# Kernel tuning notes

Hardware: AMD Instinct MI355X
Metric: run time of the kernel (lower is better)

Reference implementation:

```python
import jax, jax.numpy as jnp
import numpy as np

HIDDEN = 1024
HEADS = 16
HEAD_DIM = HIDDEN // HEADS


def setup_inputs() -> dict:
    key = jax.random.key(0)
    ks = jax.random.split(key, 8)
    B, S = 2, 2048
    scale = 1.0 / np.sqrt(HIDDEN)
    inp = {
        "hidden_states": jax.random.normal(ks[0], (B, S, HIDDEN), dtype=jnp.float32),
        "attention_mask": jnp.zeros((B, 1, 1, S), dtype=jnp.float32),
        "q_w": jax.random.normal(ks[1], (HIDDEN, HIDDEN), dtype=jnp.float32) * scale,
        "q_b": jnp.zeros((HIDDEN,), dtype=jnp.float32),
        "k_w": jax.random.normal(ks[2], (HIDDEN, HIDDEN), dtype=jnp.float32) * scale,
        "k_b": jnp.zeros((HIDDEN,), dtype=jnp.float32),
        "v_w": jax.random.normal(ks[3], (HIDDEN, HIDDEN), dtype=jnp.float32) * scale,
        "v_b": jnp.zeros((HIDDEN,), dtype=jnp.float32),
    }
    return inp


def _split_heads(x):
    # [B, S, H] -> [B, heads, S, head_dim]
    B, S, _ = x.shape
    return x.reshape(B, S, HEADS, HEAD_DIM).transpose(0, 2, 1, 3)


def reference(hidden_states, attention_mask, q_w, q_b, k_w, k_b, v_w, v_b):
    # Linear projections (torch Linear: x @ W.T + b; here weights stored as [in, out])
    q = _split_heads(hidden_states @ q_w + q_b)  # [B, h, S, d]
    k = _split_heads(hidden_states @ k_w + k_b)
    v = _split_heads(hidden_states @ v_w + v_b)

    scores = jnp.einsum("bhqd,bhkd->bhqk", q, k) / jnp.sqrt(jnp.float32(HEAD_DIM))
    scores = scores + attention_mask  # additive mask, broadcast [B,1,1,S]
    probs = jax.nn.softmax(scores, axis=-1)
    # dropout prob = 0.0 -> identity
    ctx = jnp.einsum("bhqk,bhkd->bhqd", probs, v)  # [B, h, S, d]
    B, _, S, _ = ctx.shape
    ctx = ctx.transpose(0, 2, 1, 3).reshape(B, S, HIDDEN)
    return ctx
```

## Files before the change

kernel.cpp:

```cpp
#include <hip/hip_runtime.h>

typedef __bf16 bf16;
typedef __attribute__((ext_vector_type(8))) __bf16 bf16x8;
typedef __attribute__((ext_vector_type(4))) __bf16 bf16x4;
typedef __attribute__((ext_vector_type(4))) float f32x4;

#define MFMA(a, b, c) __builtin_amdgcn_mfma_f32_16x16x32_bf16((a), (b), (c), 0, 0, 0)
#define LOG2E 1.44269504088896340736f

__device__ __forceinline__ bf16x8 cvt8(float4 a, float4 b) {
  bf16x8 r;
  r[0] = (bf16)a.x; r[1] = (bf16)a.y; r[2] = (bf16)a.z; r[3] = (bf16)a.w;
  r[4] = (bf16)b.x; r[5] = (bf16)b.y; r[6] = (bf16)b.z; r[7] = (bf16)b.w;
  return r;
}

__device__ __forceinline__ void stage16(const bf16* g, bf16* l) {
  __builtin_amdgcn_global_load_lds(
      (const __attribute__((address_space(1))) void*)g,
      (__attribute__((address_space(3))) void*)l, 16, 0, 0);
}

__global__ __launch_bounds__(256)
void cvt(const float* __restrict__ hs, const float* __restrict__ qw,
         const float* __restrict__ kw, const float* __restrict__ vw,
         bf16* __restrict__ Xb, bf16* __restrict__ Wt) {
  const int bid = blockIdx.x, tid = threadIdx.x;
  if (bid < 2048) {
    size_t off = (size_t)bid * 2048 + tid * 8;
    float4 x0 = *(const float4*)(hs + off);
    float4 x1 = *(const float4*)(hs + off + 4);
    *(bf16x8*)(Xb + off) = cvt8(x0, x1);
  } else {
    int t = bid - 2048;
    int z = t >> 8, ti = t & 255;
    const float* W = (z == 0) ? qw : (z == 1) ? kw : vw;
    int k0 = (ti >> 4) * 64, n0 = (ti & 15) * 64;
    __shared__ bf16 T[64 * 72];
    #pragma unroll
    for (int i = 0; i < 16; ++i) {
      int e = i * 256 + tid;
      int kr = e >> 6, nc = e & 63;
      T[nc * 72 + kr] = (bf16)W[(size_t)(k0 + kr) * 1024 + n0 + nc];
    }
    __syncthreads();
    #pragma unroll
    for (int i = 0; i < 2; ++i) {
      int e = i * 256 + tid;
      int nr = e >> 3, kg = e & 7;
      *(bf16x8*)(Wt + (size_t)z * 1048576 + (size_t)(n0 + nr) * 1024 + k0 + kg * 8) =
          *(const bf16x8*)&T[nr * 72 + kg * 8];
    }
  }
}

__global__ __launch_bounds__(256, 3)
void qkv_gemm(const bf16* __restrict__ Xb, const bf16* __restrict__ Wt,
              const float* __restrict__ qbias, const float* __restrict__ kbias,
              const float* __restrict__ vbias,
              bf16* __restrict__ qo, bf16* __restrict__ ko, bf16* __restrict__ vo) {
  const int blk = blockIdx.x;
  const int xcd = blk & 7, slot = blk >> 3;
  const int mb = xcd * 4 + slot / 24;
  const int nb = slot % 24;
  const int z = nb >> 3, nbm = nb & 7;
  const bf16* W = Wt + (size_t)z * 1048576;

  const int tid = threadIdx.x;
  const int wave = tid >> 6, lane = tid & 63, quad = lane >> 4, c = lane & 15;
  const int wr = wave >> 1, wc = wave & 1;
  const int lrow = lane >> 3;
  const int lg = (lane & 7) ^ lrow;

  __shared__ bf16 As[128 * 64];
  __shared__ bf16 Bs[128 * 64];

  f32x4 acc[4][4] = {};

  for (int k0 = 0; k0 < 1024; k0 += 64) {
    #pragma unroll
    for (int i = 0; i < 4; ++i) {
      int r = wave * 32 + i * 8;
      stage16(Xb + (size_t)(mb * 128 + r + lrow) * 1024 + k0 + lg * 8, &As[r * 64]);
      stage16(W + (size_t)(nbm * 128 + r + lrow) * 1024 + k0 + lg * 8, &Bs[r * 64]);
    }
    __syncthreads();
    #pragma unroll
    for (int ch = 0; ch < 2; ++ch) {
      bf16x8 af[4];
      #pragma unroll
      for (int rt = 0; rt < 4; ++rt) {
        int row = wr * 64 + rt * 16 + c;
        af[rt] = *(const bf16x8*)&As[row * 64 + ((((ch << 2) | quad) ^ (c & 7)) << 3)];
      }
      #pragma unroll
      for (int nt = 0; nt < 4; ++nt) {
        int row = wc * 64 + nt * 16 + c;
        bf16x8 bfrag = *(const bf16x8*)&Bs[row * 64 + ((((ch << 2) | quad) ^ (c & 7)) << 3)];
        #pragma unroll
        for (int rt = 0; rt < 4; ++rt)
          acc[rt][nt] = MFMA(af[rt], bfrag, acc[rt][nt]);
      }
    }
    __syncthreads();
  }

  const float* bias = (z == 0) ? qbias : (z == 1) ? kbias : vbias;
  float bv[4];
  #pragma unroll
  for (int nt = 0; nt < 4; ++nt)
    bv[nt] = bias[nbm * 128 + wc * 64 + nt * 16 + c];

  if (z == 2) {
    #pragma unroll
    for (int rt = 0; rt < 4; ++rt)
      #pragma unroll
      for (int nt = 0; nt < 4; ++nt) {
        int m0 = mb * 128 + wr * 64 + rt * 16 + 4 * quad;
        int n = nbm * 128 + wc * 64 + nt * 16 + c;
        bf16x4 pk;
        #pragma unroll
        for (int reg = 0; reg < 4; ++reg) pk[reg] = (bf16)(acc[rt][nt][reg] + bv[nt]);
        int b = m0 >> 11, s0 = m0 & 2047, h = n >> 6, d = n & 63;
        *(bf16x4*)&vo[(((size_t)b * 16 + h) * 64 + d) * 2048 + s0] = pk;
      }
  } else {
    bf16* dst = (z == 0) ? qo : ko;
    const float scale = (z == 0) ? 0.125f * LOG2E : 1.0f;
    #pragma unroll
    for (int rt = 0; rt < 4; ++rt)
      #pragma unroll
      for (int nt = 0; nt < 4; ++nt)
        #pragma unroll
        for (int reg = 0; reg < 4; ++reg) {
          float v = (acc[rt][nt][reg] + bv[nt]) * scale;
          int m = mb * 128 + wr * 64 + rt * 16 + 4 * quad + reg;
          int n = nbm * 128 + wc * 64 + nt * 16 + c;
          int b = m >> 11, s = m & 2047, h = n >> 6, d = n & 63;
          dst[(((size_t)b * 16 + h) * 2048 + s) * 64 + d] = (bf16)v;
        }
  }
}

__global__ __launch_bounds__(512, 4)
void attn(const bf16* __restrict__ qg, const bf16* __restrict__ kg,
          const bf16* __restrict__ vtg, const float* __restrict__ mask,
          float* __restrict__ out) {
  const int blk = blockIdx.x;
  const int xcd = blk & 7, slot = blk >> 3;
  const int bh = xcd * 4 + (slot >> 4);
  const int qblk = slot & 15;
  const int b = bh >> 4, h = bh & 15;
  const int tid = threadIdx.x;
  const int wave = tid >> 6, lane = tid & 63, quad = lane >> 4, c = lane & 15;
  const int lrow = lane >> 3, lg = (lane & 7) ^ lrow;

  __shared__ bf16 Ks[2][64 * 64];
  __shared__ bf16 Vs[2][64 * 64];
  __shared__ bf16 Ps[8][1024];

  const bf16* qb_ = qg + (size_t)bh * 2048 * 64;
  const bf16* kb_ = kg + (size_t)bh * 2048 * 64;
  const bf16* vb_ = vtg + (size_t)bh * 64 * 2048;

  bf16x8 qf[2];
  #pragma unroll
  for (int ch = 0; ch < 2; ++ch)
    qf[ch] = *(const bf16x8*)(qb_ +
        (size_t)(qblk * 128 + wave * 16 + c) * 64 + ch * 32 + quad * 8);

  f32x4 o[4] = {};
  float lsum = 0.f;

  {
    int r = wave * 8;
    stage16(kb_ + (size_t)(r + lrow) * 64 + lg * 8, &Ks[0][r * 64]);
    stage16(vb_ + (size_t)(r + lrow) * 2048 + lg * 8, &Vs[0][r * 64]);
  }
  __asm__ volatile("s_waitcnt vmcnt(0)" ::: "memory");
  __builtin_amdgcn_s_barrier();

  for (int kt = 0; kt < 32; ++kt) {
    const int cur = kt & 1;

    if (kt < 31) {
      int r = wave * 8;
      stage16(kb_ + (size_t)((kt + 1) * 64 + r + lrow) * 64 + lg * 8,
              &Ks[cur ^ 1][r * 64]);
      stage16(vb_ + (size_t)(r + lrow) * 2048 + (kt + 1) * 64 + lg * 8,
              &Vs[cur ^ 1][r * 64]);
    }
    __builtin_amdgcn_sched_barrier(0);

    f32x4 s[4] = {};
    #pragma unroll
    for (int nt = 0; nt < 4; ++nt)
      #pragma unroll
      for (int ch = 0; ch < 2; ++ch) {
        bf16x8 kf = *(const bf16x8*)&Ks[cur][(nt * 16 + c) * 64 +
                                            ((((ch << 2) | quad) ^ (c & 7)) << 3)];
        s[nt] = MFMA(kf, qf[ch], s[nt]);
      }

    #pragma unroll
    for (int nt = 0; nt < 4; ++nt) {
      float4 mv = *(const float4*)&mask[b * 2048 + kt * 64 + nt * 16 + 4 * quad];
      bf16x4 pk;
      #pragma unroll
      for (int reg = 0; reg < 4; ++reg) {
        float mreg = (reg == 0) ? mv.x : (reg == 1) ? mv.y : (reg == 2) ? mv.z : mv.w;
        float p = __builtin_amdgcn_exp2f(s[nt][reg] + mreg * LOG2E);
        lsum += p;
        pk[reg] = (bf16)p;
      }
      int g = (nt * 2 + (quad >> 1)) ^ (c & 7);
      *(bf16x4*)&Ps[wave][c * 64 + g * 8 + (quad & 1) * 4] = pk;
    }
    __asm__ volatile("s_waitcnt lgkmcnt(0)" ::: "memory");

    #pragma unroll
    for (int ch = 0; ch < 2; ++ch) {
      bf16x8 pa = *(const bf16x8*)&Ps[wave][c * 64 +
                                           ((((ch << 2) | quad) ^ (c & 7)) << 3)];
      #pragma unroll
      for (int nt = 0; nt < 4; ++nt) {
        bf16x8 vf = *(const bf16x8*)&Vs[cur][(nt * 16 + c) * 64 +
                                            ((((ch << 2) | quad) ^ (c & 7)) << 3)];
        o[nt] = MFMA(vf, pa, o[nt]);
      }
    }

    __asm__ volatile("s_waitcnt vmcnt(0) lgkmcnt(0)" ::: "memory");
    __builtin_amdgcn_s_barrier();
  }

  lsum += __shfl_xor(lsum, 16, 64);
  lsum += __shfl_xor(lsum, 32, 64);
  const float inv = 1.0f / lsum;

  const int srow = qblk * 128 + wave * 16 + c;
  #pragma unroll
  for (int nt = 0; nt < 4; ++nt) {
    float4 st = { o[nt][0] * inv, o[nt][1] * inv, o[nt][2] * inv, o[nt][3] * inv };
    *(float4*)&out[((size_t)b * 2048 + srow) * 1024 + h * 64 + nt * 16 + 4 * quad] = st;
  }
}

extern "C" void kernel_launch(void* const* d_in, const int* in_sizes, int n_in,
                              void* d_out, int out_size, void* d_ws, size_t ws_size,
                              hipStream_t stream) {
  const float* hs   = (const float*)d_in[0];
  const float* mask = (const float*)d_in[1];
  const float* qw   = (const float*)d_in[2];
  const float* qb   = (const float*)d_in[3];
  const float* kw   = (const float*)d_in[4];
  const float* kb   = (const float*)d_in[5];
  const float* vw   = (const float*)d_in[6];
  const float* vb   = (const float*)d_in[7];
  float* out = (float*)d_out;

  bf16* Xb   = (bf16*)d_ws;
  bf16* Wt   = Xb + (size_t)4096 * 1024;
  bf16* q_ws = Wt + (size_t)3 * 1048576;
  bf16* k_ws = q_ws + (size_t)4096 * 1024;
  bf16* v_ws = k_ws + (size_t)4096 * 1024;

  cvt<<<dim3(2816), 256, 0, stream>>>(hs, qw, kw, vw, Xb, Wt);
  qkv_gemm<<<dim3(768), 256, 0, stream>>>(Xb, Wt, qb, kb, vb, q_ws, k_ws, v_ws);
  attn<<<dim3(512), 512, 0, stream>>>(q_ws, k_ws, v_ws, mask, out);
}
```

Before: 177.0 us.

## Halve attention waves, give each wave two query tiles to reuse K/V fragments

The attention kernel now runs 4 waves per block instead of 8, and each wave handles 32 query rows as two 16-row tiles. Each K and V fragment read from LDS feeds two MFMAs, which halves LDS read traffic per unit of MFMA work, and mask loads are hoisted ahead of the QK MFMAs. The P scratch buffer is padded to a 68-element row stride and read as two 4-element halves to avoid bank conflicts. Each wave needs roughly twice the accumulator registers, and with fewer waves per block there is less latency hiding and each wave stages more loads.

After: 176.9 us. No clear change (-0.1%).

```diff
diff --git a/kernel.cpp b/kernel.cpp
--- a/kernel.cpp
+++ b/kernel.cpp
@@ -142,7 +142,7 @@
   }
 }
 
-__global__ __launch_bounds__(512, 4)
+__global__ __launch_bounds__(256, 2)
 void attn(const bf16* __restrict__ qg, const bf16* __restrict__ kg,
           const bf16* __restrict__ vtg, const float* __restrict__ mask,
           float* __restrict__ out) {
@@ -155,25 +155,28 @@
   const int wave = tid >> 6, lane = tid & 63, quad = lane >> 4, c = lane & 15;
   const int lrow = lane >> 3, lg = (lane & 7) ^ lrow;
 
-  __shared__ bf16 Ks[2][64 * 64];
-  __shared__ bf16 Vs[2][64 * 64];
-  __shared__ bf16 Ps[8][1024];
+  __shared__ __align__(16) bf16 Ks[2][64 * 64];
+  __shared__ __align__(16) bf16 Vs[2][64 * 64];
+  __shared__ __align__(16) bf16 Ps[4][2][16 * 68];
 
   const bf16* qb_ = qg + (size_t)bh * 2048 * 64;
   const bf16* kb_ = kg + (size_t)bh * 2048 * 64;
   const bf16* vb_ = vtg + (size_t)bh * 64 * 2048;
 
-  bf16x8 qf[2];
-  #pragma unroll
-  for (int ch = 0; ch < 2; ++ch)
-    qf[ch] = *(const bf16x8*)(qb_ +
-        (size_t)(qblk * 128 + wave * 16 + c) * 64 + ch * 32 + quad * 8);
-
-  f32x4 o[4] = {};
-  float lsum = 0.f;
-
-  {
-    int r = wave * 8;
+  bf16x8 qf[2][2];
+  #pragma unroll
+  for (int ct = 0; ct < 2; ++ct)
+    #pragma unroll
+    for (int ch = 0; ch < 2; ++ch)
+      qf[ct][ch] = *(const bf16x8*)(qb_ +
+          (size_t)(qblk * 128 + wave * 32 + ct * 16 + c) * 64 + ch * 32 + quad * 8);
+
+  f32x4 o[2][4] = {};
+  float lsum[2] = {0.f, 0.f};
+
+  #pragma unroll
+  for (int i = 0; i < 2; ++i) {
+    int r = wave * 16 + i * 8;
     stage16(kb_ + (size_t)(r + lrow) * 64 + lg * 8, &Ks[0][r * 64]);
     stage16(vb_ + (size_t)(r + lrow) * 2048 + lg * 8, &Vs[0][r * 64]);
   }
@@ -184,49 +187,70 @@
     const int cur = kt & 1;
 
     if (kt < 31) {
-      int r = wave * 8;
-      stage16(kb_ + (size_t)((kt + 1) * 64 + r + lrow) * 64 + lg * 8,
-              &Ks[cur ^ 1][r * 64]);
-      stage16(vb_ + (size_t)(r + lrow) * 2048 + (kt + 1) * 64 + lg * 8,
-              &Vs[cur ^ 1][r * 64]);
+      #pragma unroll
+      for (int i = 0; i < 2; ++i) {
+        int r = wave * 16 + i * 8;
+        stage16(kb_ + (size_t)((kt + 1) * 64 + r + lrow) * 64 + lg * 8,
+                &Ks[cur ^ 1][r * 64]);
+        stage16(vb_ + (size_t)(r + lrow) * 2048 + (kt + 1) * 64 + lg * 8,
+                &Vs[cur ^ 1][r * 64]);
+      }
     }
     __builtin_amdgcn_sched_barrier(0);
 
-    f32x4 s[4] = {};
+    float4 mv[4];
+    #pragma unroll
+    for (int nt = 0; nt < 4; ++nt)
+      mv[nt] = *(const float4*)&mask[b * 2048 + kt * 64 + nt * 16 + 4 * quad];
+
+    f32x4 s[2][4] = {};
     #pragma unroll
     for (int nt = 0; nt < 4; ++nt)
       #pragma unroll
       for (int ch = 0; ch < 2; ++ch) {
         bf16x8 kf = *(const bf16x8*)&Ks[cur][(nt * 16 + c) * 64 +
                                             ((((ch << 2) | quad) ^ (c & 7)) << 3)];
-        s[nt] = MFMA(kf, qf[ch], s[nt]);
-      }
-
-    #pragma unroll
-    for (int nt = 0; nt < 4; ++nt) {
-      float4 mv = *(const float4*)&mask[b * 2048 + kt * 64 + nt * 16 + 4 * quad];
-      bf16x4 pk;
-      #pragma unroll
-      for (int reg = 0; reg < 4; ++reg) {
-        float mreg = (reg == 0) ? mv.x : (reg == 1) ? mv.y : (reg == 2) ? mv.z : mv.w;
-        float p = __builtin_amdgcn_exp2f(s[nt][reg] + mreg * LOG2E);
-        lsum += p;
-        pk[reg] = (bf16)p;
-      }
-      int g = (nt * 2 + (quad >> 1)) ^ (c & 7);
-      *(bf16x4*)&Ps[wave][c * 64 + g * 8 + (quad & 1) * 4] = pk;
-    }
+        #pragma unroll
+        for (int ct = 0; ct < 2; ++ct)
+          s[ct][nt] = MFMA(kf, qf[ct][ch], s[ct][nt]);
+      }
+
+    #pragma unroll
+    for (int ct = 0; ct < 2; ++ct)
+      #pragma unroll
+      for (int nt = 0; nt < 4; ++nt) {
+        bf16x4 pk;
+        #pragma unroll
+        for (int reg = 0; reg < 4; ++reg) {
+          float mreg = (reg == 0) ? mv[nt].x : (reg == 1) ? mv[nt].y
+                     : (reg == 2) ? mv[nt].z : mv[nt].w;
+          float p = __builtin_amdgcn_exp2f(s[ct][nt][reg] + mreg * LOG2E);
+          lsum[ct] += p;
+          pk[reg] = (bf16)p;
+        }
+        int g = (nt * 2 + (quad >> 1)) ^ (c & 7);
+        *(bf16x4*)&Ps[wave][ct][c * 68 + g * 8 + (quad & 1) * 4] = pk;
+      }
     __asm__ volatile("s_waitcnt lgkmcnt(0)" ::: "memory");
 
     #pragma unroll
     for (int ch = 0; ch < 2; ++ch) {
-      bf16x8 pa = *(const bf16x8*)&Ps[wave][c * 64 +
-                                           ((((ch << 2) | quad) ^ (c & 7)) << 3)];
+      bf16x8 pa[2];
+      #pragma unroll
+      for (int ct = 0; ct < 2; ++ct) {
+        int gp = ((ch << 2) | quad) ^ (c & 7);
+        bf16x4 lo = *(const bf16x4*)&Ps[wave][ct][c * 68 + gp * 8];
+        bf16x4 hi = *(const bf16x4*)&Ps[wave][ct][c * 68 + gp * 8 + 4];
+        pa[ct][0] = lo[0]; pa[ct][1] = lo[1]; pa[ct][2] = lo[2]; pa[ct][3] = lo[3];
+        pa[ct][4] = hi[0]; pa[ct][5] = hi[1]; pa[ct][6] = hi[2]; pa[ct][7] = hi[3];
+      }
       #pragma unroll
       for (int nt = 0; nt < 4; ++nt) {
         bf16x8 vf = *(const bf16x8*)&Vs[cur][(nt * 16 + c) * 64 +
                                             ((((ch << 2) | quad) ^ (c & 7)) << 3)];
-        o[nt] = MFMA(vf, pa, o[nt]);
+        #pragma unroll
+        for (int ct = 0; ct < 2; ++ct)
+          o[ct][nt] = MFMA(vf, pa[ct], o[ct][nt]);
       }
     }
 
@@ -234,15 +258,19 @@
     __builtin_amdgcn_s_barrier();
   }
 
-  lsum += __shfl_xor(lsum, 16, 64);
-  lsum += __shfl_xor(lsum, 32, 64);
-  const float inv = 1.0f / lsum;
-
-  const int srow = qblk * 128 + wave * 16 + c;
-  #pragma unroll
-  for (int nt = 0; nt < 4; ++nt) {
-    float4 st = { o[nt][0] * inv, o[nt][1] * inv, o[nt][2] * inv, o[nt][3] * inv };
-    *(float4*)&out[((size_t)b * 2048 + srow) * 1024 + h * 64 + nt * 16 + 4 * quad] = st;
+  #pragma unroll
+  for (int ct = 0; ct < 2; ++ct) {
+    float l = lsum[ct];
+    l += __shfl_xor(l, 16, 64);
+    l += __shfl_xor(l, 32, 64);
+    const float inv = 1.0f / l;
+    const int srow = qblk * 128 + wave * 32 + ct * 16 + c;
+    #pragma unroll
+    for (int nt = 0; nt < 4; ++nt) {
+      float4 st = { o[ct][nt][0] * inv, o[ct][nt][1] * inv,
+                    o[ct][nt][2] * inv, o[ct][nt][3] * inv };
+      *(float4*)&out[((size_t)b * 2048 + srow) * 1024 + h * 64 + nt * 16 + 4 * quad] = st;
+    }
   }
 }
 
@@ -267,5 +295,5 @@
 
   cvt<<<dim3(2816), 256, 0, stream>>>(hs, qw, kw, vw, Xb, Wt);
   qkv_gemm<<<dim3(768), 256, 0, stream>>>(Xb, Wt, qb, kb, vb, q_ws, k_ws, v_ws);
-  attn<<<dim3(512), 512, 0, stream>>>(q_ws, k_ws, v_ws, mask, out);
-}
+  attn<<<dim3(512), 256, 0, stream>>>(q_ws, k_ws, v_ws, mask, out);
+}
```
